# Kernel tuning notes

Measured on AMD Instinct MI355X. Metric: run time of the kernel, lower is better.

Reference implementation:

```python
import jax, jax.numpy as jnp
import numpy as np

N_ATOMS, N_EDGES, FEAT, N_RBF, N_CONV = 20000, 320000, 128, 20, 3
CUTOFF = 5.0
ATOM_FEA, H_FEA, N_OUT, VOCAB = 64, 128, 5, 100


def _dense(x, W, b):
    return x @ W + b


def _painn_forward(xyz, embed, W1, b1, W2, b2, Wd, bd, U, V, Ws1, bs1, Ws2, bs2,
                   Wr1, br1, Wr2, br2, Wf1, bf1, Wf2, bf2, Wf3, bf3, z, nbrs):
    act = jax.nn.silu
    i_idx, j_idx = nbrs[:, 0], nbrs[:, 1]          # receiver i, sender j
    r_ij = xyz[j_idx] - xyz[i_idx]                 # [E,3]
    d = jnp.sqrt(jnp.sum(r_ij ** 2, -1) + 1e-12)   # [E]
    unit = r_ij / d[:, None]
    n = jnp.arange(1, N_RBF + 1, dtype=xyz.dtype)
    rbf = jnp.sin(n[None, :] * jnp.pi * d[:, None] / CUTOFF) / d[:, None]   # [E,n_rbf]
    f_cut = 0.5 * (jnp.cos(jnp.pi * d / CUTOFF) + 1.0) * (d < CUTOFF)       # cosine envelope

    s = embed[z]                                   # [N,F]
    v = jnp.zeros((s.shape[0], FEAT, 3), s.dtype)  # [N,F,3]

    for l in range(N_CONV):
        # ---- message block ----
        phi = _dense(act(_dense(s, W1[l], b1[l])), W2[l], b2[l])        # [N,3F]
        w_s = _dense(rbf, Wd[l], bd[l]) * f_cut[:, None]                # [E,3F]
        inv = (phi[j_idx] * w_s).reshape(-1, 3, FEAT)                   # [E,3,F]
        dv_ij = unit[:, None, :] * inv[:, 2, :, None] + inv[:, 0, :, None] * v[j_idx]  # [E,F,3]
        s = s + jax.ops.segment_sum(inv[:, 1, :], i_idx, num_segments=N_ATOMS)
        v = v + jax.ops.segment_sum(dv_ij, i_idx, num_segments=N_ATOMS)
        # ---- update block ----
        u_v = jnp.einsum('nfd,fg->ngd', v, U[l])                        # [N,F,3]
        v_v = jnp.einsum('nfd,fg->ngd', v, V[l])
        v_norm = jnp.sqrt(jnp.sum(v_v ** 2, -1) + 1e-12)                # [N,F]
        split = _dense(act(_dense(jnp.concatenate([s, v_norm], -1), Ws1[l], bs1[l])), Ws2[l], bs2[l])
        a_vv = split[:, :FEAT]
        a_sv = split[:, FEAT:2 * FEAT]
        a_ss = split[:, 2 * FEAT:]
        v = v + u_v * a_vv[:, :, None]
        s = s + jnp.sum(u_v * v_v, -1) * a_sv + a_ss

    # ---- readout (per-atom features) + fully connected head ----
    atom_fea = _dense(act(_dense(s, Wr1, br1)), Wr2, br2)               # [N,atom_fea]
    h = act(_dense(atom_fea, Wf1, bf1))
    h = act(_dense(h, Wf2, bf2))
    return _dense(h, Wf3, bf3)                                          # [N,n_outputs]


def setup_inputs() -> dict:
    key = jax.random.key(0)
    ks = jax.random.split(key, 20)
    sc = 0.08  # ~1/sqrt(feat_dim) to keep activations stable
    def rn(k, shape, s=sc):
        return jax.random.normal(k, shape, dtype=jnp.float32) * s
    return {
        'xyz': jax.random.uniform(ks[0], (N_ATOMS, 3), dtype=jnp.float32) * 4.0,
        'z': jax.random.randint(ks[1], (N_ATOMS,), 0, VOCAB),
        'nbrs': jax.random.randint(ks[2], (N_EDGES, 2), 0, N_ATOMS),
        'embed': rn(ks[3], (VOCAB, FEAT), 1.0),
        'W1': rn(ks[4], (N_CONV, FEAT, FEAT)), 'b1': jnp.zeros((N_CONV, FEAT)),
        'W2': rn(ks[5], (N_CONV, FEAT, 3 * FEAT)), 'b2': jnp.zeros((N_CONV, 3 * FEAT)),
        'Wd': rn(ks[6], (N_CONV, N_RBF, 3 * FEAT)), 'bd': jnp.zeros((N_CONV, 3 * FEAT)),
        'U': rn(ks[7], (N_CONV, FEAT, FEAT)),
        'V': rn(ks[8], (N_CONV, FEAT, FEAT)),
        'Ws1': rn(ks[9], (N_CONV, 2 * FEAT, FEAT)), 'bs1': jnp.zeros((N_CONV, FEAT)),
        'Ws2': rn(ks[10], (N_CONV, FEAT, 3 * FEAT)), 'bs2': jnp.zeros((N_CONV, 3 * FEAT)),
        'Wr1': rn(ks[11], (FEAT, FEAT)), 'br1': jnp.zeros((FEAT,)),
        'Wr2': rn(ks[12], (FEAT, ATOM_FEA)), 'br2': jnp.zeros((ATOM_FEA,)),
        'Wf1': rn(ks[13], (ATOM_FEA, H_FEA)), 'bf1': jnp.zeros((H_FEA,)),
        'Wf2': rn(ks[14], (H_FEA, H_FEA)), 'bf2': jnp.zeros((H_FEA,)),
        'Wf3': rn(ks[15], (H_FEA, N_OUT)), 'bf3': jnp.zeros((N_OUT,)),
    }


def reference(xyz, z, nbrs, embed, W1, b1, W2, b2, Wd, bd, U, V, Ws1, bs1, Ws2, bs2,
              Wr1, br1, Wr2, br2, Wf1, bf1, Wf2, bf2, Wf3, bf3):
    return _painn_forward(xyz, embed, W1, b1, W2, b2, Wd, bd, U, V, Ws1, bs1, Ws2, bs2,
                          Wr1, br1, Wr2, br2, Wf1, bf1, Wf2, bf2, Wf3, bf3, z, nbrs)
```

## Files before the change

### kernel.cpp

```cpp
#include <hip/hip_runtime.h>
#include <hip/hip_bf16.h>
#include <math.h>

#define N_ATOMS 20000
#define N_EDGES 320000
#define FEAT 128
#define N_RBF 20
#define N_CONV 3
#define N_OUT_ 5
#define PI_F 3.14159265358979f
#define M20P 20032
#define M60P 60032

typedef unsigned short ushort;
typedef __bf16 bf16x8 __attribute__((ext_vector_type(8)));
typedef float f32x4 __attribute__((ext_vector_type(4)));

__device__ __forceinline__ float b2f(ushort u){ return __uint_as_float(((unsigned)u) << 16); }
__device__ __forceinline__ ushort f2b(float x){
    unsigned u = __float_as_uint(x);
    return (ushort)((u + 0x7FFFu + ((u >> 16) & 1u)) >> 16);
}

constexpr size_t rnd64(size_t x){ return (x + 63) & ~size_t(63); }
constexpr size_t F_XYZ  = 64;
constexpr size_t F_EMB  = rnd64(F_XYZ + 60000);
constexpr size_t F_B1   = rnd64(F_EMB + 12800);
constexpr size_t F_B2   = rnd64(F_B1  + 3*128);
constexpr size_t F_WD   = rnd64(F_B2  + 3*384);
constexpr size_t F_BD   = rnd64(F_WD  + 3*20*384);
constexpr size_t F_BS1  = rnd64(F_BD  + 3*384);
constexpr size_t F_BS2  = rnd64(F_BS1 + 3*128);
constexpr size_t F_BR1  = rnd64(F_BS2 + 3*384);
constexpr size_t F_BR2  = rnd64(F_BR1 + 128);
constexpr size_t F_BF1  = rnd64(F_BR2 + 64);
constexpr size_t F_BF2  = rnd64(F_BF1 + 128);
constexpr size_t F_BF3  = rnd64(F_BF2 + 128);
constexpr size_t F_CNT  = rnd64(F_BF3 + 8);
constexpr size_t F_ROW  = rnd64(F_CNT  + N_ATOMS);
constexpr size_t F_CUR  = rnd64(F_ROW  + N_ATOMS + 1);
constexpr size_t F_EID  = rnd64(F_CUR  + N_ATOMS);
constexpr size_t F_EJ   = rnd64(F_EID  + N_EDGES);
constexpr size_t F_EREC = rnd64(F_EJ   + N_EDGES);
constexpr size_t F_S    = rnd64(F_EREC + (size_t)N_EDGES*24);
constexpr size_t F_V    = rnd64(F_S    + (size_t)N_ATOMS*FEAT);
constexpr size_t F_PHI  = rnd64(F_V    + (size_t)60000*FEAT);
constexpr size_t F_VV   = rnd64(F_PHI  + (size_t)N_ATOMS*384);
constexpr size_t F_SPL  = rnd64(F_VV   + (size_t)60000*FEAT);
constexpr size_t F_OUT  = rnd64(F_SPL  + (size_t)N_ATOMS*384);
constexpr size_t H_SHI  = rnd64(F_OUT  + N_ATOMS*N_OUT_);
constexpr size_t H_SLO  = rnd64(H_SHI  + (size_t)M20P*128/2);
constexpr size_t H_VHI  = rnd64(H_SLO  + (size_t)M20P*128/2);
constexpr size_t H_VLO  = rnd64(H_VHI  + (size_t)M60P*128/2);
constexpr size_t H_HAHI = rnd64(H_VLO  + (size_t)M60P*128/2);
constexpr size_t H_HALO = rnd64(H_HAHI + (size_t)M20P*128/2);
// ... 20 lines not shown
__global__ void k_cvt_all(P13 sp, float* __restrict__ ws, const int* __restrict__ flag){
    constexpr int   NSEG = 13;
    constexpr int    SZ[NSEG] = {60000,12800,384,1152,23040,1152,384,1152,128,64,128,128,5};
    constexpr size_t DO_[NSEG]= {F_XYZ,F_EMB,F_B1,F_B2,F_WD,F_BD,F_BS1,F_BS2,F_BR1,F_BR2,F_BF1,F_BF2,F_BF3};
    int t = blockIdx.x * blockDim.x + threadIdx.x;
    int bf = *flag;
    #pragma unroll
    for (int s = 0; s < NSEG; s++){
        if (t < SZ[s]){
            float v = bf ? b2f(((const ushort*)sp.p[s])[t]) : ((const float*)sp.p[s])[t];
            ws[DO_[s] + t] = v;
            return;
        }
        t -= SZ[s];
    }
}

struct P11 { const void* p[11]; };
__global__ void k_wt_all(P11 sp, ushort* __restrict__ wb, const int* __restrict__ flag){
    constexpr int NSEG = 23;
    constexpr int SRC[NSEG]  = {0,1,2,3,4,5, 0,1,2,3,4,5, 0,1,2,3,4,5, 6,7,8,9,10};
    constexpr int SOFF[NSEG] = {0,0,0,0,0,0, 16384,49152,16384,16384,32768,49152,
                                32768,98304,32768,32768,65536,98304, 0,0,0,0,0};
    constexpr size_t DOFF[NSEG]={O_W1T,O_W2T,O_UT,O_VT,O_WS1T,O_WS2T,
                                 O_W1T+16384,O_W2T+49152,O_UT+16384,O_VT+16384,O_WS1T+32768,O_WS2T+49152,
                                 O_W1T+32768,O_W2T+98304,O_UT+32768,O_VT+32768,O_WS1T+65536,O_WS2T+98304,
                                 O_WR1T,O_WR2T,O_WF1T,O_WF2T,O_WF3T};
    constexpr int KK[NSEG]   = {128,128,128,128,256,128, 128,128,128,128,256,128,
                                128,128,128,128,256,128, 128,128,64,128,128};
    constexpr int NN[NSEG]   = {128,384,128,128,128,384, 128,384,128,128,128,384,
                                128,384,128,128,128,384, 128,64,128,128,5};
    constexpr int NP[NSEG]   = {128,384,128,128,128,384, 128,384,128,128,128,384,
                                128,384,128,128,128,384, 128,64,128,128,64};
    int t = blockIdx.x * blockDim.x + threadIdx.x;
    int bf = *flag;
    #pragma unroll
    for (int s = 0; s < NSEG; s++){
        int tot = NP[s] * KK[s];
        if (t < tot){
            int n = t / KK[s], k = t & (KK[s] - 1);
            ushort hi = 0, lo = 0;
            if (n < NN[s]){
                int si = SOFF[s] + k * NN[s] + n;
                float w = bf ? b2f(((const ushort*)sp.p[SRC[s]])[si])
                             : ((const float*)sp.p[SRC[s]])[si];
                hi = f2b(w); lo = f2b(w - b2f(hi));
            }
            wb[DOFF[s] + t] = hi;
            wb[O_WTOT + DOFF[s] + t] = lo;
            return;
        }
        t -= tot;
    }
}
constexpr int WT_TOTAL = 598016;

__global__ void k_store_out(const float* __restrict__ src, void* __restrict__ dst, int n,
                            const int* __restrict__ flag){
    int t = blockIdx.x * blockDim.x + threadIdx.x;
    if (t >= n) return;
    float v = src[t];
    if (*flag) ((ushort*)dst)[t] = f2b(v);
    else       ((float*)dst)[t] = v;
}

__global__ void k_zero_f(float* p, int n){
    int t = blockIdx.x * blockDim.x + threadIdx.x;
    if (t < n) p[t] = 0.f;
}
__global__ void k_zero_i(int* p, int n){
    int t = blockIdx.x * blockDim.x + threadIdx.x;
    if (t < n) p[t] = 0;
}
__global__ void k_init_s(const float* __restrict__ embed, const int* __restrict__ z,
                         float* __restrict__ s, ushort* __restrict__ shi,
                         ushort* __restrict__ slo){
    int t = blockIdx.x * blockDim.x + threadIdx.x;
    if (t >= N_ATOMS * FEAT) return;
    int n = t >> 7, f = t & 127;
    float v = embed[z[n] * FEAT + f];
    s[t] = v;
    ushort h = f2b(v); shi[t] = h; slo[t] = f2b(v - b2f(h));
// ... 57 lines not shown
    }
}

template<int KT>
__global__ __launch_bounds__(256) void k_gemm3t(
    const ushort* __restrict__ Ahi, const ushort* __restrict__ Alo,
    const ushort* __restrict__ Bthi, const ushort* __restrict__ Btlo,
    const float* __restrict__ bias, int M, int N, int act,
    float* __restrict__ Cf, ushort* __restrict__ Chi, ushort* __restrict__ Clo)
{
    int wave = threadIdx.x >> 6, lane = threadIdx.x & 63;
    int l15 = lane & 15, quad = lane >> 4;
    int m0 = blockIdx.y * 128 + wave * 32;
    int n0 = blockIdx.x * 64;
    const ushort* aph = Ahi  + (size_t)(m0 + l15) * KT + quad * 8;
    const ushort* apl = Alo  + (size_t)(m0 + l15) * KT + quad * 8;
    const ushort* bph = Bthi + (size_t)(n0 + l15) * KT + quad * 8;
    const ushort* bpl = Btlo + (size_t)(n0 + l15) * KT + quad * 8;
    f32x4 acc[2][4];
    #pragma unroll
    for (int r = 0; r < 2; r++)
        #pragma unroll
        for (int c = 0; c < 4; c++) acc[r][c] = (f32x4){0.f, 0.f, 0.f, 0.f};
    #pragma unroll
    for (int k0 = 0; k0 < KT; k0 += 32) {
        bf16x8 ah0 = *reinterpret_cast<const bf16x8*>(aph + k0);
        bf16x8 al0 = *reinterpret_cast<const bf16x8*>(apl + k0);
        bf16x8 ah1 = *reinterpret_cast<const bf16x8*>(aph + (size_t)16 * KT + k0);
        bf16x8 al1 = *reinterpret_cast<const bf16x8*>(apl + (size_t)16 * KT + k0);
        #pragma unroll
        for (int c = 0; c < 4; c++) {
            bf16x8 bh = *reinterpret_cast<const bf16x8*>(bph + (size_t)c * 16 * KT + k0);
            bf16x8 bl = *reinterpret_cast<const bf16x8*>(bpl + (size_t)c * 16 * KT + k0);
            acc[0][c] = __builtin_amdgcn_mfma_f32_16x16x32_bf16(al0, bh, acc[0][c], 0, 0, 0);
            acc[0][c] = __builtin_amdgcn_mfma_f32_16x16x32_bf16(ah0, bl, acc[0][c], 0, 0, 0);
            acc[0][c] = __builtin_amdgcn_mfma_f32_16x16x32_bf16(ah0, bh, acc[0][c], 0, 0, 0);
            acc[1][c] = __builtin_amdgcn_mfma_f32_16x16x32_bf16(al1, bh, acc[1][c], 0, 0, 0);
            acc[1][c] = __builtin_amdgcn_mfma_f32_16x16x32_bf16(ah1, bl, acc[1][c], 0, 0, 0);
            acc[1][c] = __builtin_amdgcn_mfma_f32_16x16x32_bf16(ah1, bh, acc[1][c], 0, 0, 0);
        }
    }
    #pragma unroll
    for (int rr = 0; rr < 2; rr++) {
        int row_base = m0 + rr * 16 + quad * 4;
        #pragma unroll
        for (int c = 0; c < 4; c++) {
            int col = n0 + c * 16 + l15;
            #pragma unroll
            for (int r = 0; r < 4; r++) {
                int row = row_base + r;
                if (row < M && col < N) {
                    float v = acc[rr][c][r];
                    if (bias) v += bias[col];
                    if (act)  v = v / (1.f + expf(-v));
                    size_t idx = (size_t)row * N + col;
                    if (Cf)  Cf[idx] = v;
                    if (Chi) { ushort h = f2b(v); Chi[idx] = h; Clo[idx] = f2b(v - b2f(h)); }
                }
            }
        }
    }
}

__global__ __launch_bounds__(256) void k_gemm3_dual(
    const ushort* __restrict__ Ahi, const ushort* __restrict__ Alo,
    const ushort* __restrict__ B1hi, const ushort* __restrict__ B1lo,
    const ushort* __restrict__ B2hi, const ushort* __restrict__ B2lo,
    int M, float* __restrict__ C1, float* __restrict__ C2)
{
    constexpr int KT = 128, N = 128;
    int wave = threadIdx.x >> 6, lane = threadIdx.x & 63;
    int l15 = lane & 15, quad = lane >> 4;
    int m0 = blockIdx.y * 128 + wave * 32;
    int n0 = blockIdx.x * 64;
    const ushort* aph = Ahi  + (size_t)(m0 + l15) * KT + quad * 8;
    const ushort* apl = Alo  + (size_t)(m0 + l15) * KT + quad * 8;
    const ushort* b1h = B1hi + (size_t)(n0 + l15) * KT + quad * 8;
    const ushort* b1l = B1lo + (size_t)(n0 + l15) * KT + quad * 8;
    const ushort* b2h = B2hi + (size_t)(n0 + l15) * KT + quad * 8;
    const ushort* b2l = B2lo + (size_t)(n0 + l15) * KT + quad * 8;
    f32x4 acc1[2][4], acc2[2][4];
    #pragma unroll
    for (int r = 0; r < 2; r++)
        #pragma unroll
        for (int c = 0; c < 4; c++) {
            acc1[r][c] = (f32x4){0.f,0.f,0.f,0.f};
            acc2[r][c] = (f32x4){0.f,0.f,0.f,0.f};
        }
    #pragma unroll
    for (int k0 = 0; k0 < KT; k0 += 32) {
        bf16x8 ah0 = *reinterpret_cast<const bf16x8*>(aph + k0);
        bf16x8 al0 = *reinterpret_cast<const bf16x8*>(apl + k0);
        bf16x8 ah1 = *reinterpret_cast<const bf16x8*>(aph + (size_t)16 * KT + k0);
        bf16x8 al1 = *reinterpret_cast<const bf16x8*>(apl + (size_t)16 * KT + k0);
        #pragma unroll
        for (int c = 0; c < 4; c++) {
            bf16x8 bh = *reinterpret_cast<const bf16x8*>(b1h + (size_t)c * 16 * KT + k0);
            bf16x8 bl = *reinterpret_cast<const bf16x8*>(b1l + (size_t)c * 16 * KT + k0);
            acc1[0][c] = __builtin_amdgcn_mfma_f32_16x16x32_bf16(al0, bh, acc1[0][c], 0, 0, 0);
            acc1[0][c] = __builtin_amdgcn_mfma_f32_16x16x32_bf16(ah0, bl, acc1[0][c], 0, 0, 0);
            acc1[0][c] = __builtin_amdgcn_mfma_f32_16x16x32_bf16(ah0, bh, acc1[0][c], 0, 0, 0);
            acc1[1][c] = __builtin_amdgcn_mfma_f32_16x16x32_bf16(al1, bh, acc1[1][c], 0, 0, 0);
            acc1[1][c] = __builtin_amdgcn_mfma_f32_16x16x32_bf16(ah1, bl, acc1[1][c], 0, 0, 0);
            acc1[1][c] = __builtin_amdgcn_mfma_f32_16x16x32_bf16(ah1, bh, acc1[1][c], 0, 0, 0);
        }
        #pragma unroll
        for (int c = 0; c < 4; c++) {
            bf16x8 bh = *reinterpret_cast<const bf16x8*>(b2h + (size_t)c * 16 * KT + k0);
            bf16x8 bl = *reinterpret_cast<const bf16x8*>(b2l + (size_t)c * 16 * KT + k0);
            acc2[0][c] = __builtin_amdgcn_mfma_f32_16x16x32_bf16(al0, bh, acc2[0][c], 0, 0, 0);
            acc2[0][c] = __builtin_amdgcn_mfma_f32_16x16x32_bf16(ah0, bl, acc2[0][c], 0, 0, 0);
            acc2[0][c] = __builtin_amdgcn_mfma_f32_16x16x32_bf16(ah0, bh, acc2[0][c], 0, 0, 0);
            acc2[1][c] = __builtin_amdgcn_mfma_f32_16x16x32_bf16(al1, bh, acc2[1][c], 0, 0, 0);
            acc2[1][c] = __builtin_amdgcn_mfma_f32_16x16x32_bf16(ah1, bl, acc2[1][c], 0, 0, 0);
            acc2[1][c] = __builtin_amdgcn_mfma_f32_16x16x32_bf16(ah1, bh, acc2[1][c], 0, 0, 0);
        }
    }
    #pragma unroll
    for (int rr = 0; rr < 2; rr++) {
        int row_base = m0 + rr * 16 + quad * 4;
        #pragma unroll
        for (int c = 0; c < 4; c++) {
            int col = n0 + c * 16 + l15;
            #pragma unroll
            for (int r = 0; r < 4; r++) {
                int row = row_base + r;
                if (row < M) {
                    size_t idx = (size_t)row * N + col;
                    C1[idx] = acc1[rr][c][r];
                    C2[idx] = acc2[rr][c][r];
                }
            }
        }
    }
}

__global__ __launch_bounds__(128) void k_edge4(
    const float* __restrict__ phi, const float* __restrict__ vin,
    const int* __restrict__ EJ, const float* __restrict__ EREC,
    const int* __restrict__ row,
    const float* __restrict__ Wd, const float* __restrict__ bd,
    float* __restrict__ s, ushort* __restrict__ vhi, ushort* __restrict__ vlo)
{
    int i = blockIdx.x, f = threadIdx.x;
    float wdr[3 * N_RBF];
    #pragma unroll
    for (int r = 0; r < N_RBF; r++) {
        wdr[r]           = Wd[r*384 + f];
        wdr[N_RBF + r]   = Wd[r*384 + 128 + f];
        wdr[2*N_RBF + r] = Wd[r*384 + 256 + f];
    }
    float bd0 = bd[f], bd1 = bd[128 + f], bd2 = bd[256 + f];
    float sacc = 0.f, va0 = 0.f, va1 = 0.f, va2 = 0.f;
    int beg = row[i], end = row[i + 1];

    auto body = [&](int idx){
        int j = EJ[idx];
        const float4* rq = reinterpret_cast<const float4*>(EREC + (size_t)idx * 24);
        float4 q0 = rq[0], q1 = rq[1], q2 = rq[2], q3 = rq[3], q4 = rq[4], q5 = rq[5];
        float g[20] = {q1.x,q1.y,q1.z,q1.w, q2.x,q2.y,q2.z,q2.w,
                       q3.x,q3.y,q3.z,q3.w, q4.x,q4.y,q4.z,q4.w,
                       q5.x,q5.y,q5.z,q5.w};
        float w0 = bd0 * q0.x, w1 = bd1 * q0.x, w2 = bd2 * q0.x;
        #pragma unroll
        for (int r = 0; r < N_RBF; r++) {
            w0 = fmaf(g[r], wdr[r],           w0);
            w1 = fmaf(g[r], wdr[N_RBF + r],   w1);
            w2 = fmaf(g[r], wdr[2*N_RBF + r], w2);
        }
        size_t pj = (size_t)j * 384;
        float inv0 = phi[pj + f]       * w0;
        float inv1 = phi[pj + 128 + f] * w1;
        float inv2 = phi[pj + 256 + f] * w2;
        size_t vj = (size_t)j * 384 + f;
        sacc += inv1;
        va0 = fmaf(inv0, vin[vj],       fmaf(q0.y, inv2, va0));
        va1 = fmaf(inv0, vin[vj + 128], fmaf(q0.z, inv2, va1));
        va2 = fmaf(inv0, vin[vj + 256], fmaf(q0.w, inv2, va2));
    };

    int idx = beg;
    for (; idx + 1 < end; idx += 2) { body(idx); body(idx + 1); }
    if (idx < end) body(idx);

    s[(size_t)i * FEAT + f] += sacc;
    size_t vi = (size_t)i * 384 + f;
    float n0 = vin[vi] + va0, n1 = vin[vi + 128] + va1, n2 = vin[vi + 256] + va2;
    ushort h;
    h = f2b(n0); vhi[vi]       = h; vlo[vi]       = f2b(n0 - b2f(h));
    h = f2b(n1); vhi[vi + 128] = h; vlo[vi + 128] = f2b(n1 - b2f(h));
    h = f2b(n2); vhi[vi + 256] = h; vlo[vi + 256] = f2b(n2 - b2f(h));
}

__global__ void k_vnorm_cat(const float* __restrict__ s, const float* __restrict__ vv,
                            ushort* __restrict__ chi, ushort* __restrict__ clo){
    int t = blockIdx.x * blockDim.x + threadIdx.x;
    if (t >= N_ATOMS * FEAT) return;
    int n = t >> 7, g = t & 127;
    size_t b = (size_t)n * 384 + g;
    float a0 = vv[b], a1 = vv[b + 128], a2 = vv[b + 256];
    float nr = sqrtf(a0*a0 + a1*a1 + a2*a2 + 1e-12f);
    float sv = s[t];
    size_t c0 = (size_t)n * 256 + g;
    ushort h;
    h = f2b(sv); chi[c0]       = h; clo[c0]       = f2b(sv - b2f(h));
    h = f2b(nr); chi[c0 + 128] = h; clo[c0 + 128] = f2b(nr - b2f(h));
}

__global__ void k_update(const float* __restrict__ uv, const float* __restrict__ vv,
                         const float* __restrict__ spl,
                         const ushort* __restrict__ vhi, const ushort* __restrict__ vlo,
                         float* __restrict__ s, float* __restrict__ v,
                         ushort* __restrict__ shi, ushort* __restrict__ slo){
    int t = blockIdx.x * blockDim.x + threadIdx.x;
    if (t >= N_ATOMS * FEAT) return;
    int n = t >> 7, g = t & 127;
    size_t sp = (size_t)n * 384 + g;
    float avv = spl[sp], asv = spl[sp + 128], ass = spl[sp + 256];
    float dot = 0.f;
    size_t b = (size_t)n * 384 + g;
    #pragma unroll
    for (int d = 0; d < 3; d++) {
        size_t idx = b + (size_t)d * 128;
        float u  = uv[idx];
        float w  = vv[idx];
        float vb = b2f(vhi[idx]) + b2f(vlo[idx]);
        dot = fmaf(u, w, dot);
        v[idx] = vb + u * avv;
    }
    float ns = s[t] + dot * asv + ass;
    s[t] = ns;
    ushort h = f2b(ns); shi[t] = h; slo[t] = f2b(ns - b2f(h));
}

struct Pair { ushort* hi; ushort* lo; };

static inline void gemm3(Pair A, Pair B, const float* bias,
                         int M, int K, int N, int Npad, int act,
                         float* Cf, Pair C, hipStream_t s){
    dim3 g(Npad / 64, (M + 127) / 128), b(256);
    switch (K) {
    case 64:  k_gemm3t<64> <<<g, b, 0, s>>>(A.hi, A.lo, B.hi, B.lo, bias, M, N, act, Cf, C.hi, C.lo); break;
    case 128: k_gemm3t<128><<<g, b, 0, s>>>(A.hi, A.lo, B.hi, B.lo, bias, M, N, act, Cf, C.hi, C.lo); break;
    case 256: k_gemm3t<256><<<g, b, 0, s>>>(A.hi, A.lo, B.hi, B.lo, bias, M, N, act, Cf, C.hi, C.lo); break;
    }
}

extern "C" void kernel_launch(void* const* d_in, const int* in_sizes, int n_in,
                              void* d_out, int out_size, void* d_ws, size_t ws_size,
                              hipStream_t stream) {
    float* ws = (float*)d_ws;
    int* flag = (int*)d_ws;
    const int* z    = (const int*)d_in[1];
    const int* nbrs = (const int*)d_in[2];

    k_detect<<<1, 64, 0, stream>>>((const unsigned int*)d_in[0], flag);

    P13 cp; {
        const int cidx[13] = {0,3,5,7,8,9,13,15,17,19,21,23,25};
        for (int i = 0; i < 13; i++) cp.p[i] = d_in[cidx[i]];
    }
    k_cvt_all<<<(100517 + 255)/256, 256, 0, stream>>>(cp, ws, flag);

    ushort* wb = (ushort*)(ws + H_WT);
    P11 wp; {
        const int widx[11] = {4,6,10,11,12,14,16,18,20,22,24};
        for (int i = 0; i < 11; i++) wp.p[i] = d_in[widx[i]];
    }
    k_wt_all<<<(WT_TOTAL + 255)/256, 256, 0, stream>>>(wp, wb, flag);

    int* cnt = (int*)(ws + F_CNT); int* row = (int*)(ws + F_ROW);
    int* cur = (int*)(ws + F_CUR); int* eid = (int*)(ws + F_EID);
    int* EJ  = (int*)(ws + F_EJ);  float* EREC = ws + F_EREC;
    k_zero_i<<<(N_ATOMS+255)/256, 256, 0, stream>>>(cnt, N_ATOMS);
    k_hist<<<(N_EDGES+255)/256, 256, 0, stream>>>(nbrs, cnt);
    k_scan<<<1, 256, 0, stream>>>(cnt, row, cur);
    k_fill<<<(N_EDGES+255)/256, 256, 0, stream>>>(nbrs, cur, eid);
    k_geom_csr<<<(N_EDGES+255)/256, 256, 0, stream>>>(ws + F_XYZ, nbrs, eid, EJ, EREC);

    float* S   = ws + F_S;
    float* V   = ws + F_V;
    float* PHI = ws + F_PHI;
    float* VV  = ws + F_VV;
    float* SPL = ws + F_SPL;
    auto WPW = [&](size_t off){ return Pair{ wb + off, wb + O_WTOT + off }; };
    Pair SHL { (ushort*)(ws + H_SHI),  (ushort*)(ws + H_SLO)  };
    Pair VHL { (ushort*)(ws + H_VHI),  (ushort*)(ws + H_VLO)  };
    Pair HA  { (ushort*)(ws + H_HAHI), (ushort*)(ws + H_HALO) };
    Pair HB  { (ushort*)(ws + H_HBHI), (ushort*)(ws + H_HBLO) };
    Pair AF  { (ushort*)(ws + H_AFHI), (ushort*)(ws + H_AFLO) };
    Pair CAT { (ushort*)(ws + F_SPL),  (ushort*)(ws + F_SPL) + (size_t)M20P*256 };
    Pair NOP { nullptr, nullptr };

    k_init_s<<<(N_ATOMS*FEAT+255)/256, 256, 0, stream>>>(ws + F_EMB, z, S, SHL.hi, SHL.lo);
    k_zero_f<<<(60000*FEAT+255)/256, 256, 0, stream>>>(V, 60000*FEAT);

    for (int l = 0; l < N_CONV; l++) {
        gemm3(SHL, WPW(O_W1T + l*16384), ws + F_B1 + l*128, N_ATOMS, 128, 128, 128, 1, nullptr, HA, stream);
        gemm3(HA,  WPW(O_W2T + l*49152), ws + F_B2 + l*384, N_ATOMS, 128, 384, 384, 0, PHI, NOP, stream);
        k_edge4<<<N_ATOMS, 128, 0, stream>>>(PHI, V, EJ, EREC, row,
                                             ws + F_WD + (size_t)l*20*384, ws + F_BD + l*384,
                                             S, VHL.hi, VHL.lo);
        {
            dim3 g(2, (60000 + 127) / 128), b(256);
            k_gemm3_dual<<<g, b, 0, stream>>>(VHL.hi, VHL.lo,
                                              wb + O_UT + l*16384, wb + O_WTOT + O_UT + l*16384,
                                              wb + O_VT + l*16384, wb + O_WTOT + O_VT + l*16384,
                                              60000, PHI, VV);
        }
        k_vnorm_cat<<<(N_ATOMS*FEAT+255)/256, 256, 0, stream>>>(S, VV, CAT.hi, CAT.lo);
        gemm3(CAT, WPW(O_WS1T + l*32768), ws + F_BS1 + l*128, N_ATOMS, 256, 128, 128, 1, nullptr, HB, stream);
        gemm3(HB,  WPW(O_WS2T + l*49152), ws + F_BS2 + l*384, N_ATOMS, 128, 384, 384, 0, SPL, NOP, stream);
        k_update<<<(N_ATOMS*FEAT+255)/256, 256, 0, stream>>>(PHI, VV, SPL, VHL.hi, VHL.lo,
                                                             S, V, SHL.hi, SHL.lo);
    }

    gemm3(SHL, WPW(O_WR1T), ws + F_BR1, N_ATOMS, 128, 128, 128, 1, nullptr, HA, stream);
    gemm3(HA,  WPW(O_WR2T), ws + F_BR2, N_ATOMS, 128,  64,  64, 0, nullptr, AF, stream);
    gemm3(AF,  WPW(O_WF1T), ws + F_BF1, N_ATOMS,  64, 128, 128, 1, nullptr, HB, stream);
    gemm3(HB,  WPW(O_WF2T), ws + F_BF2, N_ATOMS, 128, 128, 128, 1, nullptr, HA, stream);
    gemm3(HA,  WPW(O_WF3T), ws + F_BF3, N_ATOMS, 128, N_OUT_, 64, 0, ws + F_OUT, NOP, stream);

    k_store_out<<<(N_ATOMS*N_OUT_+255)/256, 256, 0, stream>>>(ws + F_OUT, d_out, N_ATOMS*N_OUT_, flag);
}
```

Before: 1.361 ms.

## Fuse consecutive MLP GEMM pairs through LDS-resident hidden activations

Adds a fused two-layer GEMM kernel in which each 96-row block computes the first dense+SiLU layer into shared memory as hi/lo bf16 pairs, then runs the second dense layer straight from LDS. The per-layer message and update MLPs and the readout/head pairs now use it, which removes the global round trip for the hidden activations and cuts the number of kernel launches. Separately, the edge loop unroll goes from 2 to 4. The fused kernel uses 192-thread blocks and about 52KB of LDS, which may lower occupancy. Each block also re-reads the full weight matrices from global memory without staging them in LDS.

Result: slower. 1.449 ms (+6.5%).

```diff
diff --git a/kernel.cpp b/kernel.cpp
--- a/kernel.cpp
+++ b/kernel.cpp
@@ -21,6 +21,7 @@
     unsigned u = __float_as_uint(x);
     return (ushort)((u + 0x7FFFu + ((u >> 16) & 1u)) >> 16);
 }
+#define MFMA __builtin_amdgcn_mfma_f32_16x16x32_bf16
 
 constexpr size_t rnd64(size_t x){ return (x + 63) & ~size_t(63); }
 constexpr size_t F_XYZ  = 64;
@@ -246,12 +247,12 @@
         for (int c = 0; c < 4; c++) {
             bf16x8 bh = *reinterpret_cast<const bf16x8*>(bph + (size_t)c * 16 * KT + k0);
             bf16x8 bl = *reinterpret_cast<const bf16x8*>(bpl + (size_t)c * 16 * KT + k0);
-            acc[0][c] = __builtin_amdgcn_mfma_f32_16x16x32_bf16(al0, bh, acc[0][c], 0, 0, 0);
-            acc[0][c] = __builtin_amdgcn_mfma_f32_16x16x32_bf16(ah0, bl, acc[0][c], 0, 0, 0);
-            acc[0][c] = __builtin_amdgcn_mfma_f32_16x16x32_bf16(ah0, bh, acc[0][c], 0, 0, 0);
-            acc[1][c] = __builtin_amdgcn_mfma_f32_16x16x32_bf16(al1, bh, acc[1][c], 0, 0, 0);
-            acc[1][c] = __builtin_amdgcn_mfma_f32_16x16x32_bf16(ah1, bl, acc[1][c], 0, 0, 0);
-            acc[1][c] = __builtin_amdgcn_mfma_f32_16x16x32_bf16(ah1, bh, acc[1][c], 0, 0, 0);
+            acc[0][c] = MFMA(al0, bh, acc[0][c], 0, 0, 0);
+            acc[0][c] = MFMA(ah0, bl, acc[0][c], 0, 0, 0);
+            acc[0][c] = MFMA(ah0, bh, acc[0][c], 0, 0, 0);
+            acc[1][c] = MFMA(al1, bh, acc[1][c], 0, 0, 0);
+            acc[1][c] = MFMA(ah1, bl, acc[1][c], 0, 0, 0);
+            acc[1][c] = MFMA(ah1, bh, acc[1][c], 0, 0, 0);
         }
     }
     #pragma unroll
@@ -270,6 +271,121 @@
                     size_t idx = (size_t)row * N + col;
                     if (Cf)  Cf[idx] = v;
                     if (Chi) { ushort h = f2b(v); Chi[idx] = h; Clo[idx] = f2b(v - b2f(h)); }
+                }
+            }
+        }
+    }
+}
+
+template<int K1, int N2, int ACT2>
+__global__ __launch_bounds__(192) void k_fused2(
+    const ushort* __restrict__ Ahi, const ushort* __restrict__ Alo,
+    const ushort* __restrict__ B1hi, const ushort* __restrict__ B1lo,
+    const float* __restrict__ bias1,
+    const ushort* __restrict__ B2hi, const ushort* __restrict__ B2lo,
+    const float* __restrict__ bias2,
+    int M, float* __restrict__ Cf, ushort* __restrict__ Chi, ushort* __restrict__ Clo)
+{
+    constexpr int LDH = 136;
+    __shared__ ushort hH[96 * LDH];
+    __shared__ ushort hL[96 * LDH];
+    int wave = threadIdx.x >> 6, lane = threadIdx.x & 63;
+    int l15 = lane & 15, quad = lane >> 4;
+    int m0 = blockIdx.x * 96 + wave * 32;
+
+    {
+        const ushort* aph = Ahi  + (size_t)(m0 + l15) * K1 + quad * 8;
+        const ushort* apl = Alo  + (size_t)(m0 + l15) * K1 + quad * 8;
+        const ushort* bph = B1hi + (size_t)l15 * K1 + quad * 8;
+        const ushort* bpl = B1lo + (size_t)l15 * K1 + quad * 8;
+        f32x4 acc[2][8];
+        #pragma unroll
+        for (int r = 0; r < 2; r++)
+            #pragma unroll
+            for (int c = 0; c < 8; c++) acc[r][c] = (f32x4){0.f,0.f,0.f,0.f};
+        #pragma unroll
+        for (int k0 = 0; k0 < K1; k0 += 32) {
+            bf16x8 ah0 = *reinterpret_cast<const bf16x8*>(aph + k0);
+            bf16x8 al0 = *reinterpret_cast<const bf16x8*>(apl + k0);
+            bf16x8 ah1 = *reinterpret_cast<const bf16x8*>(aph + (size_t)16 * K1 + k0);
+            bf16x8 al1 = *reinterpret_cast<const bf16x8*>(apl + (size_t)16 * K1 + k0);
+            #pragma unroll
+            for (int c = 0; c < 8; c++) {
+                bf16x8 bh = *reinterpret_cast<const bf16x8*>(bph + (size_t)c * 16 * K1 + k0);
+                bf16x8 bl = *reinterpret_cast<const bf16x8*>(bpl + (size_t)c * 16 * K1 + k0);
+                acc[0][c] = MFMA(al0, bh, acc[0][c], 0, 0, 0);
+                acc[0][c] = MFMA(ah0, bl, acc[0][c], 0, 0, 0);
+                acc[0][c] = MFMA(ah0, bh, acc[0][c], 0, 0, 0);
+                acc[1][c] = MFMA(al1, bh, acc[1][c], 0, 0, 0);
+                acc[1][c] = MFMA(ah1, bl, acc[1][c], 0, 0, 0);
+                acc[1][c] = MFMA(ah1, bh, acc[1][c], 0, 0, 0);
+            }
+        }
+        #pragma unroll
+        for (int rr = 0; rr < 2; rr++) {
+            #pragma unroll
+            for (int c = 0; c < 8; c++) {
+                #pragma unroll
+                for (int r = 0; r < 4; r++) {
+                    int lrow = wave * 32 + rr * 16 + quad * 4 + r;
+                    int col  = c * 16 + l15;
+                    float v = acc[rr][c][r] + bias1[col];
+                    v = v / (1.f + expf(-v));
+                    ushort h = f2b(v);
+                    hH[lrow * LDH + col] = h;
+                    hL[lrow * LDH + col] = f2b(v - b2f(h));
+                }
+            }
+        }
+    }
+    __syncthreads();
+
+    constexpr int CF  = (N2 >= 128) ? 8 : N2 / 16;
+    constexpr int NCH = N2 / (CF * 16);
+    #pragma unroll 1
+    for (int ch = 0; ch < NCH; ch++) {
+        f32x4 acc[2][CF];
+        #pragma unroll
+        for (int r = 0; r < 2; r++)
+            #pragma unroll
+            for (int c = 0; c < CF; c++) acc[r][c] = (f32x4){0.f,0.f,0.f,0.f};
+        #pragma unroll
+        for (int k0 = 0; k0 < 128; k0 += 32) {
+            int arow = wave * 32 + l15;
+            bf16x8 ah0 = *reinterpret_cast<const bf16x8*>(&hH[arow * LDH + k0 + quad * 8]);
+            bf16x8 al0 = *reinterpret_cast<const bf16x8*>(&hL[arow * LDH + k0 + quad * 8]);
+            bf16x8 ah1 = *reinterpret_cast<const bf16x8*>(&hH[(arow + 16) * LDH + k0 + quad * 8]);
+            bf16x8 al1 = *reinterpret_cast<const bf16x8*>(&hL[(arow + 16) * LDH + k0 + quad * 8]);
+            #pragma unroll
+            for (int c = 0; c < CF; c++) {
+                const ushort* b2h = B2hi + (size_t)(ch * 128 + c * 16 + l15) * 128 + k0 + quad * 8;
+                const ushort* b2l = B2lo + (size_t)(ch * 128 + c * 16 + l15) * 128 + k0 + quad * 8;
+                bf16x8 bh = *reinterpret_cast<const bf16x8*>(b2h);
+                bf16x8 bl = *reinterpret_cast<const bf16x8*>(b2l);
+                acc[0][c] = MFMA(al0, bh, acc[0][c], 0, 0, 0);
+                acc[0][c] = MFMA(ah0, bl, acc[0][c], 0, 0, 0);
+                acc[0][c] = MFMA(ah0, bh, acc[0][c], 0, 0, 0);
+                acc[1][c] = MFMA(al1, bh, acc[1][c], 0, 0, 0);
+                acc[1][c] = MFMA(ah1, bl, acc[1][c], 0, 0, 0);
+                acc[1][c] = MFMA(ah1, bh, acc[1][c], 0, 0, 0);
+            }
+        }
+        #pragma unroll
+        for (int rr = 0; rr < 2; rr++) {
+            int row_base = m0 + rr * 16 + quad * 4;
+            #pragma unroll
+            for (int c = 0; c < CF; c++) {
+                int col = ch * 128 + c * 16 + l15;
+                #pragma unroll
+                for (int r = 0; r < 4; r++) {
+                    int row = row_base + r;
+                    if (row < M) {
+                        float v = acc[rr][c][r] + bias2[col];
+                        if (ACT2) v = v / (1.f + expf(-v));
+                        size_t idx = (size_t)row * N2 + col;
+                        if (Cf)  Cf[idx] = v;
+                        if (Chi) { ushort h = f2b(v); Chi[idx] = h; Clo[idx] = f2b(v - b2f(h)); }
+                    }
                 }
             }
         }
@@ -311,23 +427,23 @@
         for (int c = 0; c < 4; c++) {
             bf16x8 bh = *reinterpret_cast<const bf16x8*>(b1h + (size_t)c * 16 * KT + k0);
             bf16x8 bl = *reinterpret_cast<const bf16x8*>(b1l + (size_t)c * 16 * KT + k0);
-            acc1[0][c] = __builtin_amdgcn_mfma_f32_16x16x32_bf16(al0, bh, acc1[0][c], 0, 0, 0);
-            acc1[0][c] = __builtin_amdgcn_mfma_f32_16x16x32_bf16(ah0, bl, acc1[0][c], 0, 0, 0);
-            acc1[0][c] = __builtin_amdgcn_mfma_f32_16x16x32_bf16(ah0, bh, acc1[0][c], 0, 0, 0);
-            acc1[1][c] = __builtin_amdgcn_mfma_f32_16x16x32_bf16(al1, bh, acc1[1][c], 0, 0, 0);
-            acc1[1][c] = __builtin_amdgcn_mfma_f32_16x16x32_bf16(ah1, bl, acc1[1][c], 0, 0, 0);
-            acc1[1][c] = __builtin_amdgcn_mfma_f32_16x16x32_bf16(ah1, bh, acc1[1][c], 0, 0, 0);
+            acc1[0][c] = MFMA(al0, bh, acc1[0][c], 0, 0, 0);
+            acc1[0][c] = MFMA(ah0, bl, acc1[0][c], 0, 0, 0);
+            acc1[0][c] = MFMA(ah0, bh, acc1[0][c], 0, 0, 0);
+            acc1[1][c] = MFMA(al1, bh, acc1[1][c], 0, 0, 0);
+            acc1[1][c] = MFMA(ah1, bl, acc1[1][c], 0, 0, 0);
+            acc1[1][c] = MFMA(ah1, bh, acc1[1][c], 0, 0, 0);
         }
         #pragma unroll
         for (int c = 0; c < 4; c++) {
             bf16x8 bh = *reinterpret_cast<const bf16x8*>(b2h + (size_t)c * 16 * KT + k0);
             bf16x8 bl = *reinterpret_cast<const bf16x8*>(b2l + (size_t)c * 16 * KT + k0);
-            acc2[0][c] = __builtin_amdgcn_mfma_f32_16x16x32_bf16(al0, bh, acc2[0][c], 0, 0, 0);
-            acc2[0][c] = __builtin_amdgcn_mfma_f32_16x16x32_bf16(ah0, bl, acc2[0][c], 0, 0, 0);
-            acc2[0][c] = __builtin_amdgcn_mfma_f32_16x16x32_bf16(ah0, bh, acc2[0][c], 0, 0, 0);
-            acc2[1][c] = __builtin_amdgcn_mfma_f32_16x16x32_bf16(al1, bh, acc2[1][c], 0, 0, 0);
-            acc2[1][c] = __builtin_amdgcn_mfma_f32_16x16x32_bf16(ah1, bl, acc2[1][c], 0, 0, 0);
-            acc2[1][c] = __builtin_amdgcn_mfma_f32_16x16x32_bf16(ah1, bh, acc2[1][c], 0, 0, 0);
+            acc2[0][c] = MFMA(al0, bh, acc2[0][c], 0, 0, 0);
+            acc2[0][c] = MFMA(ah0, bl, acc2[0][c], 0, 0, 0);
+            acc2[0][c] = MFMA(ah0, bh, acc2[0][c], 0, 0, 0);
+            acc2[1][c] = MFMA(al1, bh, acc2[1][c], 0, 0, 0);
+            acc2[1][c] = MFMA(ah1, bl, acc2[1][c], 0, 0, 0);
+            acc2[1][c] = MFMA(ah1, bh, acc2[1][c], 0, 0, 0);
         }
     }
     #pragma unroll
@@ -394,8 +510,8 @@
     };
 
     int idx = beg;
-    for (; idx + 1 < end; idx += 2) { body(idx); body(idx + 1); }
-    if (idx < end) body(idx);
+    for (; idx + 3 < end; idx += 4) { body(idx); body(idx+1); body(idx+2); body(idx+3); }
+    for (; idx < end; idx++) body(idx);
 
     s[(size_t)i * FEAT + f] += sacc;
     size_t vi = (size_t)i * 384 + f;
@@ -497,11 +613,9 @@
     float* PHI = ws + F_PHI;
     float* VV  = ws + F_VV;
     float* SPL = ws + F_SPL;
-    auto WPW = [&](size_t off){ return Pair{ wb + off, wb + O_WTOT + off }; };
     Pair SHL { (ushort*)(ws + H_SHI),  (ushort*)(ws + H_SLO)  };
     Pair VHL { (ushort*)(ws + H_VHI),  (ushort*)(ws + H_VLO)  };
     Pair HA  { (ushort*)(ws + H_HAHI), (ushort*)(ws + H_HALO) };
-    Pair HB  { (ushort*)(ws + H_HBHI), (ushort*)(ws + H_HBLO) };
     Pair AF  { (ushort*)(ws + H_AFHI), (ushort*)(ws + H_AFLO) };
     Pair CAT { (ushort*)(ws + F_SPL),  (ushort*)(ws + F_SPL) + (size_t)M20P*256 };
     Pair NOP { nullptr, nullptr };
@@ -509,9 +623,13 @@
     k_init_s<<<(N_ATOMS*FEAT+255)/256, 256, 0, stream>>>(ws + F_EMB, z, S, SHL.hi, SHL.lo);
     k_zero_f<<<(60000*FEAT+255)/256, 256, 0, stream>>>(V, 60000*FEAT);
 
+    dim3 gF((N_ATOMS + 95)/96), bF(192);
     for (int l = 0; l < N_CONV; l++) {
-        gemm3(SHL, WPW(O_W1T + l*16384), ws + F_B1 + l*128, N_ATOMS, 128, 128, 128, 1, nullptr, HA, stream);
-        gemm3(HA,  WPW(O_W2T + l*49152), ws + F_B2 + l*384, N_ATOMS, 128, 384, 384, 0, PHI, NOP, stream);
+        k_fused2<128,384,0><<<gF, bF, 0, stream>>>(
+            SHL.hi, SHL.lo,
+            wb + O_W1T + l*16384, wb + O_WTOT + O_W1T + l*16384, ws + F_B1 + l*128,
+            wb + O_W2T + l*49152, wb + O_WTOT + O_W2T + l*49152, ws + F_B2 + l*384,
+            N_ATOMS, PHI, nullptr, nullptr);
         k_edge4<<<N_ATOMS, 128, 0, stream>>>(PHI, V, EJ, EREC, row,
                                              ws + F_WD + (size_t)l*20*384, ws + F_BD + l*384,
                                              S, VHL.hi, VHL.lo);
@@ -523,17 +641,27 @@
                                               60000, PHI, VV);
         }
         k_vnorm_cat<<<(N_ATOMS*FEAT+255)/256, 256, 0, stream>>>(S, VV, CAT.hi, CAT.lo);
-        gemm3(CAT, WPW(O_WS1T + l*32768), ws + F_BS1 + l*128, N_ATOMS, 256, 128, 128, 1, nullptr, HB, stream);
-        gemm3(HB,  WPW(O_WS2T + l*49152), ws + F_BS2 + l*384, N_ATOMS, 128, 384, 384, 0, SPL, NOP, stream);
+        k_fused2<256,384,0><<<gF, bF, 0, stream>>>(
+            CAT.hi, CAT.lo,
+            wb + O_WS1T + l*32768, wb + O_WTOT + O_WS1T + l*32768, ws + F_BS1 + l*128,
+            wb + O_WS2T + l*49152, wb + O_WTOT + O_WS2T + l*49152, ws + F_BS2 + l*384,
+            N_ATOMS, SPL, nullptr, nullptr);
         k_update<<<(N_ATOMS*FEAT+255)/256, 256, 0, stream>>>(PHI, VV, SPL, VHL.hi, VHL.lo,
                                                              S, V, SHL.hi, SHL.lo);
     }
 
-    gemm3(SHL, WPW(O_WR1T), ws + F_BR1, N_ATOMS, 128, 128, 128, 1, nullptr, HA, stream);
-    gemm3(HA,  WPW(O_WR2T), ws + F_BR2, N_ATOMS, 128,  64,  64, 0, nullptr, AF, stream);
-    gemm3(AF,  WPW(O_WF1T), ws + F_BF1, N_ATOMS,  64, 128, 128, 1, nullptr, HB, stream);
-    gemm3(HB,  WPW(O_WF2T), ws + F_BF2, N_ATOMS, 128, 128, 128, 1, nullptr, HA, stream);
-    gemm3(HA,  WPW(O_WF3T), ws + F_BF3, N_ATOMS, 128, N_OUT_, 64, 0, ws + F_OUT, NOP, stream);
+    k_fused2<128,64,0><<<gF, bF, 0, stream>>>(
+        SHL.hi, SHL.lo,
+        wb + O_WR1T, wb + O_WTOT + O_WR1T, ws + F_BR1,
+        wb + O_WR2T, wb + O_WTOT + O_WR2T, ws + F_BR2,
+        N_ATOMS, nullptr, AF.hi, AF.lo);
+    k_fused2<64,128,1><<<gF, bF, 0, stream>>>(
+        AF.hi, AF.lo,
+        wb + O_WF1T, wb + O_WTOT + O_WF1T, ws + F_BF1,
+        wb + O_WF2T, wb + O_WTOT + O_WF2T, ws + F_BF2,
+        N_ATOMS, nullptr, HA.hi, HA.lo);
+    gemm3(HA, Pair{wb + O_WF3T, wb + O_WTOT + O_WF3T}, ws + F_BF3,
+          N_ATOMS, 128, N_OUT_, 64, 0, ws + F_OUT, NOP, stream);
 
     k_store_out<<<(N_ATOMS*N_OUT_+255)/256, 256, 0, stream>>>(ws + F_OUT, d_out, N_ATOMS*N_OUT_, flag);
 }
```

## Fuse Ws2 GEMM with update elementwise kernel via permuted weight layout

Applied to the files above, without the earlier changes.

The Ws2 GEMM now runs inside a new kernel that also applies the PaiNN update. Its weights are permuted at setup so each block computes the matching a_vv/a_sv/a_ss columns for a 64-feature slice. The results are staged in shared memory and applied to v and s in the same kernel, which removes the SPL round-trip to global memory and one launch per layer. In exchange the kernel holds a large shared-memory tile (about 51KB) and relies on a non-obvious column permutation.

Result: no change. 1.343 ms (-1.3%).

```diff
diff --git a/kernel.cpp b/kernel.cpp
--- a/kernel.cpp
+++ b/kernel.cpp
@@ -21,6 +21,7 @@
     unsigned u = __float_as_uint(x);
     return (ushort)((u + 0x7FFFu + ((u >> 16) & 1u)) >> 16);
 }
+#define MFMA __builtin_amdgcn_mfma_f32_16x16x32_bf16
 
 constexpr size_t rnd64(size_t x){ return (x + 63) & ~size_t(63); }
 constexpr size_t F_XYZ  = 64;
@@ -107,6 +108,7 @@
                                 128,384,128,128,128,384, 128,64,128,128,5};
     constexpr int NP[NSEG]   = {128,384,128,128,128,384, 128,384,128,128,128,384,
                                 128,384,128,128,128,384, 128,64,128,128,64};
+    constexpr int PM[NSEG]   = {0,0,0,0,0,1, 0,0,0,0,0,1, 0,0,0,0,0,1, 0,0,0,0,0};
     int t = blockIdx.x * blockDim.x + threadIdx.x;
     int bf = *flag;
     #pragma unroll
@@ -121,8 +123,11 @@
                              : ((const float*)sp.p[SRC[s]])[si];
                 hi = f2b(w); lo = f2b(w - b2f(hi));
             }
-            wb[DOFF[s] + t] = hi;
-            wb[O_WTOT + DOFF[s] + t] = lo;
+            int dr = n;
+            if (PM[s]) { int g = n & 127, tg = n >> 7; dr = (g >> 6) * 192 + tg * 64 + (g & 63); }
+            size_t di = DOFF[s] + (size_t)dr * KK[s] + k;
+            wb[di] = hi;
+            wb[O_WTOT + di] = lo;
             return;
         }
         t -= tot;
@@ -246,12 +251,12 @@
         for (int c = 0; c < 4; c++) {
             bf16x8 bh = *reinterpret_cast<const bf16x8*>(bph + (size_t)c * 16 * KT + k0);
             bf16x8 bl = *reinterpret_cast<const bf16x8*>(bpl + (size_t)c * 16 * KT + k0);
-            acc[0][c] = __builtin_amdgcn_mfma_f32_16x16x32_bf16(al0, bh, acc[0][c], 0, 0, 0);
-            acc[0][c] = __builtin_amdgcn_mfma_f32_16x16x32_bf16(ah0, bl, acc[0][c], 0, 0, 0);
-            acc[0][c] = __builtin_amdgcn_mfma_f32_16x16x32_bf16(ah0, bh, acc[0][c], 0, 0, 0);
-            acc[1][c] = __builtin_amdgcn_mfma_f32_16x16x32_bf16(al1, bh, acc[1][c], 0, 0, 0);
-            acc[1][c] = __builtin_amdgcn_mfma_f32_16x16x32_bf16(ah1, bl, acc[1][c], 0, 0, 0);
-            acc[1][c] = __builtin_amdgcn_mfma_f32_16x16x32_bf16(ah1, bh, acc[1][c], 0, 0, 0);
+            acc[0][c] = MFMA(al0, bh, acc[0][c], 0, 0, 0);
+            acc[0][c] = MFMA(ah0, bl, acc[0][c], 0, 0, 0);
+            acc[0][c] = MFMA(ah0, bh, acc[0][c], 0, 0, 0);
+            acc[1][c] = MFMA(al1, bh, acc[1][c], 0, 0, 0);
+            acc[1][c] = MFMA(ah1, bl, acc[1][c], 0, 0, 0);
+            acc[1][c] = MFMA(ah1, bh, acc[1][c], 0, 0, 0);
         }
     }
     #pragma unroll
@@ -311,23 +316,23 @@
         for (int c = 0; c < 4; c++) {
             bf16x8 bh = *reinterpret_cast<const bf16x8*>(b1h + (size_t)c * 16 * KT + k0);
             bf16x8 bl = *reinterpret_cast<const bf16x8*>(b1l + (size_t)c * 16 * KT + k0);
-            acc1[0][c] = __builtin_amdgcn_mfma_f32_16x16x32_bf16(al0, bh, acc1[0][c], 0, 0, 0);
-            acc1[0][c] = __builtin_amdgcn_mfma_f32_16x16x32_bf16(ah0, bl, acc1[0][c], 0, 0, 0);
-            acc1[0][c] = __builtin_amdgcn_mfma_f32_16x16x32_bf16(ah0, bh, acc1[0][c], 0, 0, 0);
-            acc1[1][c] = __builtin_amdgcn_mfma_f32_16x16x32_bf16(al1, bh, acc1[1][c], 0, 0, 0);
-            acc1[1][c] = __builtin_amdgcn_mfma_f32_16x16x32_bf16(ah1, bl, acc1[1][c], 0, 0, 0);
-            acc1[1][c] = __builtin_amdgcn_mfma_f32_16x16x32_bf16(ah1, bh, acc1[1][c], 0, 0, 0);
+            acc1[0][c] = MFMA(al0, bh, acc1[0][c], 0, 0, 0);
+            acc1[0][c] = MFMA(ah0, bl, acc1[0][c], 0, 0, 0);
+            acc1[0][c] = MFMA(ah0, bh, acc1[0][c], 0, 0, 0);
+            acc1[1][c] = MFMA(al1, bh, acc1[1][c], 0, 0, 0);
+            acc1[1][c] = MFMA(ah1, bl, acc1[1][c], 0, 0, 0);
+            acc1[1][c] = MFMA(ah1, bh, acc1[1][c], 0, 0, 0);
         }
         #pragma unroll
         for (int c = 0; c < 4; c++) {
             bf16x8 bh = *reinterpret_cast<const bf16x8*>(b2h + (size_t)c * 16 * KT + k0);
             bf16x8 bl = *reinterpret_cast<const bf16x8*>(b2l + (size_t)c * 16 * KT + k0);
-            acc2[0][c] = __builtin_amdgcn_mfma_f32_16x16x32_bf16(al0, bh, acc2[0][c], 0, 0, 0);
-            acc2[0][c] = __builtin_amdgcn_mfma_f32_16x16x32_bf16(ah0, bl, acc2[0][c], 0, 0, 0);
-            acc2[0][c] = __builtin_amdgcn_mfma_f32_16x16x32_bf16(ah0, bh, acc2[0][c], 0, 0, 0);
-            acc2[1][c] = __builtin_amdgcn_mfma_f32_16x16x32_bf16(al1, bh, acc2[1][c], 0, 0, 0);
-            acc2[1][c] = __builtin_amdgcn_mfma_f32_16x16x32_bf16(ah1, bl, acc2[1][c], 0, 0, 0);
-            acc2[1][c] = __builtin_amdgcn_mfma_f32_16x16x32_bf16(ah1, bh, acc2[1][c], 0, 0, 0);
+            acc2[0][c] = MFMA(al0, bh, acc2[0][c], 0, 0, 0);
+            acc2[0][c] = MFMA(ah0, bl, acc2[0][c], 0, 0, 0);
+            acc2[0][c] = MFMA(ah0, bh, acc2[0][c], 0, 0, 0);
+            acc2[1][c] = MFMA(al1, bh, acc2[1][c], 0, 0, 0);
+            acc2[1][c] = MFMA(ah1, bl, acc2[1][c], 0, 0, 0);
+            acc2[1][c] = MFMA(ah1, bh, acc2[1][c], 0, 0, 0);
         }
     }
     #pragma unroll
@@ -346,6 +351,89 @@
                 }
             }
         }
+    }
+}
+
+__global__ __launch_bounds__(384) void k_ws2up(
+    const ushort* __restrict__ Ahi, const ushort* __restrict__ Alo,
+    const ushort* __restrict__ Bphi, const ushort* __restrict__ Bplo,
+    const float* __restrict__ bs2,
+    const float* __restrict__ uv, const float* __restrict__ vvf,
+    const ushort* __restrict__ vhi, const ushort* __restrict__ vlo,
+    float* __restrict__ s, float* __restrict__ v,
+    ushort* __restrict__ shi, ushort* __restrict__ slo, int M)
+{
+    constexpr int KT = 128, LDG = 200;
+    __shared__ float gl[64 * LDG];
+    int wave = threadIdx.x >> 6, lane = threadIdx.x & 63;
+    int l15 = lane & 15, quad = lane >> 4;
+    int tg = wave >> 1, rh = wave & 1;
+    int m0 = blockIdx.y * 64 + rh * 32;
+    int X  = blockIdx.x;
+    const ushort* aph = Ahi  + (size_t)(m0 + l15) * KT + quad * 8;
+    const ushort* apl = Alo  + (size_t)(m0 + l15) * KT + quad * 8;
+    const ushort* bph = Bphi + (size_t)(X * 192 + tg * 64 + l15) * KT + quad * 8;
+    const ushort* bpl = Bplo + (size_t)(X * 192 + tg * 64 + l15) * KT + quad * 8;
+    f32x4 acc[2][4];
+    #pragma unroll
+    for (int r = 0; r < 2; r++)
+        #pragma unroll
+        for (int c = 0; c < 4; c++) acc[r][c] = (f32x4){0.f, 0.f, 0.f, 0.f};
+    #pragma unroll
+    for (int k0 = 0; k0 < KT; k0 += 32) {
+        bf16x8 ah0 = *reinterpret_cast<const bf16x8*>(aph + k0);
+        bf16x8 al0 = *reinterpret_cast<const bf16x8*>(apl + k0);
+        bf16x8 ah1 = *reinterpret_cast<const bf16x8*>(aph + (size_t)16 * KT + k0);
+        bf16x8 al1 = *reinterpret_cast<const bf16x8*>(apl + (size_t)16 * KT + k0);
+        #pragma unroll
+        for (int c = 0; c < 4; c++) {
+            bf16x8 bh = *reinterpret_cast<const bf16x8*>(bph + (size_t)c * 16 * KT + k0);
+            bf16x8 bl = *reinterpret_cast<const bf16x8*>(bpl + (size_t)c * 16 * KT + k0);
+            acc[0][c] = MFMA(al0, bh, acc[0][c], 0, 0, 0);
+            acc[0][c] = MFMA(ah0, bl, acc[0][c], 0, 0, 0);
+            acc[0][c] = MFMA(ah0, bh, acc[0][c], 0, 0, 0);
+            acc[1][c] = MFMA(al1, bh, acc[1][c], 0, 0, 0);
+            acc[1][c] = MFMA(ah1, bl, acc[1][c], 0, 0, 0);
+            acc[1][c] = MFMA(ah1, bh, acc[1][c], 0, 0, 0);
+        }
+    }
+    #pragma unroll
+    for (int rr = 0; rr < 2; rr++) {
+        #pragma unroll
+        for (int c = 0; c < 4; c++) {
+            #pragma unroll
+            for (int r = 0; r < 4; r++) {
+                int lrow = rh * 32 + rr * 16 + quad * 4 + r;
+                int gc   = c * 16 + l15;
+                gl[lrow * LDG + tg * 64 + gc] = acc[rr][c][r] + bs2[tg * 128 + X * 64 + gc];
+            }
+        }
+    }
+    __syncthreads();
+    int a0 = blockIdx.y * 64;
+    for (int t = threadIdx.x; t < 64 * 64; t += 384) {
+        int al = t >> 6, gc = t & 63;
+        int a = a0 + al;
+        if (a >= M) continue;
+        int g = X * 64 + gc;
+        float avv = gl[al * LDG + gc];
+        float asv = gl[al * LDG + 64 + gc];
+        float ass = gl[al * LDG + 128 + gc];
+        size_t b = (size_t)a * 384 + g;
+        float dot = 0.f;
+        #pragma unroll
+        for (int d = 0; d < 3; d++) {
+            size_t idx = b + (size_t)d * 128;
+            float u  = uv[idx];
+            float w  = vvf[idx];
+            float vb = b2f(vhi[idx]) + b2f(vlo[idx]);
+            dot = fmaf(u, w, dot);
+            v[idx] = vb + u * avv;
+        }
+        size_t st = (size_t)a * FEAT + g;
+        float ns = s[st] + dot * asv + ass;
+        s[st] = ns;
+        ushort h = f2b(ns); shi[st] = h; slo[st] = f2b(ns - b2f(h));
     }
 }
 
@@ -421,32 +509,6 @@
     h = f2b(nr); chi[c0 + 128] = h; clo[c0 + 128] = f2b(nr - b2f(h));
 }
 
-__global__ void k_update(const float* __restrict__ uv, const float* __restrict__ vv,
-                         const float* __restrict__ spl,
-                         const ushort* __restrict__ vhi, const ushort* __restrict__ vlo,
-                         float* __restrict__ s, float* __restrict__ v,
-                         ushort* __restrict__ shi, ushort* __restrict__ slo){
-    int t = blockIdx.x * blockDim.x + threadIdx.x;
-    if (t >= N_ATOMS * FEAT) return;
-    int n = t >> 7, g = t & 127;
-    size_t sp = (size_t)n * 384 + g;
-    float avv = spl[sp], asv = spl[sp + 128], ass = spl[sp + 256];
-    float dot = 0.f;
-    size_t b = (size_t)n * 384 + g;
-    #pragma unroll
-    for (int d = 0; d < 3; d++) {
-        size_t idx = b + (size_t)d * 128;
-        float u  = uv[idx];
-        float w  = vv[idx];
-        float vb = b2f(vhi[idx]) + b2f(vlo[idx]);
-        dot = fmaf(u, w, dot);
-        v[idx] = vb + u * avv;
-    }
-    float ns = s[t] + dot * asv + ass;
-    s[t] = ns;
-    ushort h = f2b(ns); shi[t] = h; slo[t] = f2b(ns - b2f(h));
-}
-
 struct Pair { ushort* hi; ushort* lo; };
 
 static inline void gemm3(Pair A, Pair B, const float* bias,
@@ -496,8 +558,6 @@
     float* V   = ws + F_V;
     float* PHI = ws + F_PHI;
     float* VV  = ws + F_VV;
-    float* SPL = ws + F_SPL;
-    auto WPW = [&](size_t off){ return Pair{ wb + off, wb + O_WTOT + off }; };
     Pair SHL { (ushort*)(ws + H_SHI),  (ushort*)(ws + H_SLO)  };
     Pair VHL { (ushort*)(ws + H_VHI),  (ushort*)(ws + H_VLO)  };
     Pair HA  { (ushort*)(ws + H_HAHI), (ushort*)(ws + H_HALO) };
@@ -510,8 +570,10 @@
     k_zero_f<<<(60000*FEAT+255)/256, 256, 0, stream>>>(V, 60000*FEAT);
 
     for (int l = 0; l < N_CONV; l++) {
-        gemm3(SHL, WPW(O_W1T + l*16384), ws + F_B1 + l*128, N_ATOMS, 128, 128, 128, 1, nullptr, HA, stream);
-        gemm3(HA,  WPW(O_W2T + l*49152), ws + F_B2 + l*384, N_ATOMS, 128, 384, 384, 0, PHI, NOP, stream);
+        gemm3(SHL, Pair{wb + O_W1T + l*16384, wb + O_WTOT + O_W1T + l*16384},
+              ws + F_B1 + l*128, N_ATOMS, 128, 128, 128, 1, nullptr, HA, stream);
+        gemm3(HA, Pair{wb + O_W2T + l*49152, wb + O_WTOT + O_W2T + l*49152},
+              ws + F_B2 + l*384, N_ATOMS, 128, 384, 384, 0, PHI, NOP, stream);
         k_edge4<<<N_ATOMS, 128, 0, stream>>>(PHI, V, EJ, EREC, row,
                                              ws + F_WD + (size_t)l*20*384, ws + F_BD + l*384,
                                              S, VHL.hi, VHL.lo);
@@ -523,17 +585,28 @@
                                               60000, PHI, VV);
         }
         k_vnorm_cat<<<(N_ATOMS*FEAT+255)/256, 256, 0, stream>>>(S, VV, CAT.hi, CAT.lo);
-        gemm3(CAT, WPW(O_WS1T + l*32768), ws + F_BS1 + l*128, N_ATOMS, 256, 128, 128, 1, nullptr, HB, stream);
-        gemm3(HB,  WPW(O_WS2T + l*49152), ws + F_BS2 + l*384, N_ATOMS, 128, 384, 384, 0, SPL, NOP, stream);
-        k_update<<<(N_ATOMS*FEAT+255)/256, 256, 0, stream>>>(PHI, VV, SPL, VHL.hi, VHL.lo,
-                                                             S, V, SHL.hi, SHL.lo);
-    }
-
-    gemm3(SHL, WPW(O_WR1T), ws + F_BR1, N_ATOMS, 128, 128, 128, 1, nullptr, HA, stream);
-    gemm3(HA,  WPW(O_WR2T), ws + F_BR2, N_ATOMS, 128,  64,  64, 0, nullptr, AF, stream);
-    gemm3(AF,  WPW(O_WF1T), ws + F_BF1, N_ATOMS,  64, 128, 128, 1, nullptr, HB, stream);
-    gemm3(HB,  WPW(O_WF2T), ws + F_BF2, N_ATOMS, 128, 128, 128, 1, nullptr, HA, stream);
-    gemm3(HA,  WPW(O_WF3T), ws + F_BF3, N_ATOMS, 128, N_OUT_, 64, 0, ws + F_OUT, NOP, stream);
+        gemm3(CAT, Pair{wb + O_WS1T + l*32768, wb + O_WTOT + O_WS1T + l*32768},
+              ws + F_BS1 + l*128, N_ATOMS, 256, 128, 128, 1, nullptr, HB, stream);
+        {
+            dim3 g(2, (N_ATOMS + 63) / 64), b(384);
+            k_ws2up<<<g, b, 0, stream>>>(HB.hi, HB.lo,
+                                         wb + O_WS2T + l*49152, wb + O_WTOT + O_WS2T + l*49152,
+                                         ws + F_BS2 + l*384,
+                                         PHI, VV, VHL.hi, VHL.lo,
+                                         S, V, SHL.hi, SHL.lo, N_ATOMS);
+        }
+    }
+
+    gemm3(SHL, Pair{wb + O_WR1T, wb + O_WTOT + O_WR1T}, ws + F_BR1,
+          N_ATOMS, 128, 128, 128, 1, nullptr, HA, stream);
+    gemm3(HA,  Pair{wb + O_WR2T, wb + O_WTOT + O_WR2T}, ws + F_BR2,
+          N_ATOMS, 128,  64,  64, 0, nullptr, AF, stream);
+    gemm3(AF,  Pair{wb + O_WF1T, wb + O_WTOT + O_WF1T}, ws + F_BF1,
+          N_ATOMS,  64, 128, 128, 1, nullptr, HB, stream);
+    gemm3(HB,  Pair{wb + O_WF2T, wb + O_WTOT + O_WF2T}, ws + F_BF2,
+          N_ATOMS, 128, 128, 128, 1, nullptr, HA, stream);
+    gemm3(HA,  Pair{wb + O_WF3T, wb + O_WTOT + O_WF3T}, ws + F_BF3,
+          N_ATOMS, 128, N_OUT_, 64, 0, ws + F_OUT, NOP, stream);
 
     k_store_out<<<(N_ATOMS*N_OUT_+255)/256, 256, 0, stream>>>(ws + F_OUT, d_out, N_ATOMS*N_OUT_, flag);
 }
```
